# Optimization experiments

Measured on AMD Instinct MI355X. Metric: run time of the kernel, lower is better.

## Reference

```python
import jax, jax.numpy as jnp
from jax import lax
import numpy as np

B, CIN, COUT, H, W = 16, 128, 256, 64, 64
E, K, RED = 4, 3, 4

def setup_inputs() -> dict:
    key = jax.random.key(0)
    ks = jax.random.split(key, 16)
    s = 0.05
    return {
        'x': jax.random.normal(ks[0], (B, CIN, H, W), jnp.float32),
        'expert_w': jax.random.normal(ks[1], (E, COUT, CIN, K, K), jnp.float32) * s,
        'r1_w': jax.random.normal(ks[2], (E // 2, CIN), jnp.float32) * s,
        'r1_b': jnp.zeros((E // 2,), jnp.float32),
        'r2_w': jax.random.normal(ks[3], (E, E // 2), jnp.float32) * s,
        'r2_b': jnp.zeros((E,), jnp.float32),
        'r3_w': jax.random.normal(ks[4], (E, E), jnp.float32) * s,
        'r3_b': jnp.zeros((E,), jnp.float32),
        'ca1_w': jax.random.normal(ks[5], (COUT // RED, COUT), jnp.float32) * s,
        'ca1_b': jnp.zeros((COUT // RED,), jnp.float32),
        'ca2_w': jax.random.normal(ks[6], (COUT, COUT // RED), jnp.float32) * s,
        'ca2_b': jnp.zeros((COUT,), jnp.float32),
        'sa_w': jax.random.normal(ks[7], (1, COUT, 7, 7), jnp.float32) * s,
        'sa_b': jnp.zeros((1,), jnp.float32),
        'bn_gamma': jnp.ones((COUT,), jnp.float32),
        'bn_beta': jnp.zeros((COUT,), jnp.float32),
    }

def _conv(x, w, stride, pad):
    return lax.conv_general_dilated(x, w, (stride, stride), [(pad, pad), (pad, pad)],
                                     dimension_numbers=('NCHW', 'OIHW', 'NCHW'))

def reference(x, expert_w, r1_w, r1_b, r2_w, r2_b, r3_w, r3_b,
              ca1_w, ca1_b, ca2_w, ca2_b, sa_w, sa_b, bn_gamma, bn_beta):
    # --- routing: GAP -> 1x1 convs (as matmuls) -> softmax over experts ---
    g = x.mean(axis=(2, 3))                                   # [B, Cin]
    h = jax.nn.relu(g @ r1_w.T + r1_b)
    h = jax.nn.relu(h @ r2_w.T + r2_b)
    rw = jax.nn.softmax(h @ r3_w.T + r3_b, axis=1)            # [B, E]
    # --- all experts as one stacked conv, then weighted combine ---
    w = expert_w.reshape(E * COUT, CIN, K, K)
    y = _conv(x, w, 1, 1)                                     # [B, E*Cout, H, W]
    y = y.reshape(x.shape[0], E, COUT, y.shape[2], y.shape[3])
    out = jnp.einsum('be,bechw->bchw', rw, y)                 # [B, Cout, H, W]
    # --- channel attention (SE) ---
    p = out.mean(axis=(2, 3))                                  # [B, Cout]
    ca = jax.nn.sigmoid(jax.nn.relu(p @ ca1_w.T + ca1_b) @ ca2_w.T + ca2_b)
    # --- spatial attention: 7x7 conv -> sigmoid ---
    sa = jax.nn.sigmoid(_conv(out, sa_w, 1, 3) + sa_b[None, :, None, None])  # [B,1,H,W]
    out = out * ca[:, :, None, None] * sa
    # --- BatchNorm (training mode: batch statistics) + ReLU ---
    mean = out.mean(axis=(0, 2, 3))
    var = out.var(axis=(0, 2, 3))
    out = (out - mean[None, :, None, None]) * lax.rsqrt(var + 1e-5)[None, :, None, None]
    out = out * bn_gamma[None, :, None, None] + bn_beta[None, :, None, None]
    return jax.nn.relu(out)
```

## Files before the change

kernel.cpp:

```cpp
#include <hip/hip_runtime.h>
#include <math.h>

#define B_    16
#define CIN_  128
#define COUT_ 256
#define H_    64
#define W_    64
#define HW_   4096

typedef __attribute__((ext_vector_type(8))) short short8v;
typedef __attribute__((ext_vector_type(4))) float f32x4;

#define WS_GPX     0
#define WS_RW      131072
#define WS_CP      131136
#define WS_CA      196672
#define WS_BNSCALE 208960
#define WS_BNSHIFT 209216
#define WS_SA      209472
#define WS_WSA     275008
#define WS_WCB_F   283200
#define WS_XT_F    2642496
#define WS_U_F     WS_XT_F
#define WS_MIX_F   7103040

static __device__ __forceinline__ unsigned short f2bf(float f) {
    union { float f; unsigned int u; } v; v.f = f;
    unsigned int u = v.u;
    return (unsigned short)((u + 0x7FFFu + ((u >> 16) & 1u)) >> 16);
}
static __device__ __forceinline__ float bf2f(unsigned short h) {
    union { unsigned int u; float f; } v; v.u = ((unsigned int)h) << 16;
    return v.f;
}

__device__ __forceinline__ void gl16(const void* g, const void* l) {
    __builtin_amdgcn_global_load_lds(
        (const __attribute__((address_space(1))) unsigned int*)g,
        (__attribute__((address_space(3))) unsigned int*)l, 16, 0, 0);
}

__global__ __launch_bounds__(256) void k_xt(const float* __restrict__ x,
                                            unsigned short* __restrict__ xt,
                                            float* __restrict__ gpart) {
    int wg = blockIdx.x + (blockIdx.y << 6);
    int nw = ((wg & 7) << 7) + (wg >> 3);
    int h = nw & 63, b = nw >> 6;
    int t = threadIdx.x;
    int w = t & 63, c8 = t >> 6;
    unsigned short* xtb = xt + (size_t)b * 66*66*128;
    unsigned short* orow = xtb + (((size_t)(h+1))*66 + (w+1))*128;
    float* gp = gpart + ((size_t)b*64 + h)*128;
    #pragma unroll
    for (int i = 0; i < 4; ++i) {
        int ci0 = i*32 + c8*8;
        float f[8];
        short8v vv;
        #pragma unroll
        for (int j = 0; j < 8; ++j) {
            f[j] = x[(((size_t)b*CIN_ + ci0 + j)*H_ + h)*W_ + w];
            vv[j] = (short)f2bf(f[j]);
        }
        *(short8v*)(orow + ci0) = vv;
        #pragma unroll
        for (int j = 0; j < 8; ++j) {
            float s = f[j];
            s += __shfl_down(s, 32, 64);
            s += __shfl_down(s, 16, 64);
            s += __shfl_down(s, 8, 64);
            s += __shfl_down(s, 4, 64);
            s += __shfl_down(s, 2, 64);
            s += __shfl_down(s, 1, 64);
            f[j] = s;
        }
        if (w == 0) {
            #pragma unroll
            for (int j = 0; j < 8; ++j) gp[ci0 + j] = f[j];
        }
    }
    xtb[(((size_t)(h+1))*66 + (t >> 7)*65)*128 + (t & 127)] = 0;
    if (h == 0 || h == 63) {
        int r = (h == 0) ? 0 : 65;
        unsigned short* rowp = xtb + ((size_t)r*66)*128;
        for (int i = t; i < 1056; i += 256)
            *(short8v*)(rowp + (size_t)i*8) = (short8v){0,0,0,0,0,0,0,0};
    }
}

__global__ void k_route(const float* __restrict__ gpart,
                        const float* r1w, const float* r1b,
                        const float* r2w, const float* r2b,
                        const float* r3w, const float* r3b,
                        float* __restrict__ rw) {
    int b = blockIdx.x;
    int t = threadIdx.x;
    __shared__ float gl_[128];
    float s = 0.f;
    for (int h = 0; h < 64; ++h) s += gpart[((size_t)b*64 + h)*128 + t];
    gl_[t] = s * (1.f/4096.f);
    __syncthreads();
    if (t == 0) {
        float h1[2];
        for (int j = 0; j < 2; ++j) {
            float acc = r1b[j];
            for (int c = 0; c < CIN_; ++c) acc += gl_[c]*r1w[j*CIN_+c];
            h1[j] = fmaxf(acc, 0.f);
        }
        float h2[4];
        for (int e = 0; e < 4; ++e)
            h2[e] = fmaxf(r2b[e] + h1[0]*r2w[e*2] + h1[1]*r2w[e*2+1], 0.f);
        float lg[4], m = -1e30f;
        for (int e = 0; e < 4; ++e) {
            float acc = r3b[e];
            for (int j = 0; j < 4; ++j) acc += h2[j]*r3w[e*4+j];
            lg[e] = acc; m = fmaxf(m, acc);
        }
        float den = 0.f;
        for (int e = 0; e < 4; ++e) { lg[e] = expf(lg[e]-m); den += lg[e]; }
        float inv = 1.f/den;
        for (int e = 0; e < 4; ++e) rw[b*4+e] = lg[e]*inv;
    }
}

__global__ __launch_bounds__(256) void k_wcomb(const float* __restrict__ ew,
                                               const float* __restrict__ rw,
                                               unsigned short* __restrict__ wc,
                                               const float* __restrict__ saw,
                                               unsigned short* __restrict__ wsa) {
    int t = threadIdx.x;
    if (blockIdx.x >= COUT_) {
        int i = (blockIdx.x - COUT_)*256 + t;
        int tap = i >> 8, c = i & 255;
        float v = (tap < 49) ? saw[c*49 + tap] : 0.f;
        wsa[tap*256 + c] = f2bf(v);
        return;
    }
    int co = blockIdx.x;
    __shared__ float ewl[4*1152];
    __shared__ float rwl[64];
    #pragma unroll
    for (int e = 0; e < 4; ++e) {
        const float* src = ew + ((size_t)(e*COUT_ + co))*1152;
        for (int i = t; i < 1152; i += 256) ewl[e*1152 + i] = src[i];
    }
    if (t < 64) rwl[t] = rw[t];
    __syncthreads();
    for (int i = 0; i < 72; ++i) {
        int f = i*256 + t;
        int b = f / 1152;
        int rem = f - b*1152;
        int tap = rem >> 7, ci = rem & 127;
        int lidx = ci*9 + tap;
        float v = rwl[b*4+0]*ewl[0*1152+lidx] + rwl[b*4+1]*ewl[1*1152+lidx]
                + rwl[b*4+2]*ewl[2*1152+lidx] + rwl[b*4+3]*ewl[3*1152+lidx];
        wc[((size_t)(b*9 + tap)*COUT_ + co)*128 + ci] = f2bf(v);
    }
}

__global__ __launch_bounds__(256) void k_conv(const unsigned short* __restrict__ xt,
                                              const unsigned short* __restrict__ wc,
                                              unsigned short* __restrict__ mixb,
                                              float* __restrict__ cpart) {
    __shared__ __align__(16) unsigned short xs[1600*8];
    __shared__ __align__(16) unsigned short wl[2304*8];
    __shared__ float gsl[4][64];
    int wg = blockIdx.x + (blockIdx.y << 4) + (blockIdx.z << 6);
    int nw = ((wg & 7) << 7) + (wg >> 3);
    int ht = nw & 15;
    int cb = (nw >> 4) & 3;
    int b  = nw >> 6;
    int t  = threadIdx.x;
    int wv = t >> 6, lane = t & 63;
    int lr = lane & 15, kq = lane >> 4;
    int h0 = ht * 4;

    const unsigned short* xtb = xt + (size_t)b * 66*66*128;
    const unsigned short* wcb = wc + (size_t)b * 9*256*128;

    const char* xs_c = (const char*)xs;
    const char* wl_c = (const char*)wl;
    int base_x = wv*4224 + kq*1056 + lr*16;
    int base_w = kq*1024 + lr*16;

    f32x4 acc[4][4];
    #pragma unroll
    for (int m = 0; m < 4; ++m)
        #pragma unroll
        for (int n = 0; n < 4; ++n) acc[m][n] = (f32x4){0.f,0.f,0.f,0.f};

    for (int ci0 = 0; ci0 < CIN_; ci0 += 32) {
        __syncthreads();
        for (int j = wv; j < 25; j += 4) {
            int s = j*64 + lane;
            if (s > 1583) s = 1583;
            int row = s / 264;
            int rem = s - row*264;
            int kq2 = rem / 66, col = rem - kq2*66;
            const unsigned short* g = xtb + (((size_t)(h0 + row)*66 + col)*128 + ci0 + kq2*8);
            gl16(g, (const char*)xs + (size_t)j*1024);
        }
        for (int j = wv; j < 36; j += 4) {
            int s = j*64 + lane;
            int tap = s >> 8, kq2 = (s >> 6) & 3, co = s & 63;
            const unsigned short* g = wcb + (((size_t)tap*COUT_ + cb*64 + co)*128 + ci0 + kq2*8);
            gl16(g, (const char*)wl + (size_t)j*1024);
        }
        asm volatile("s_waitcnt vmcnt(0)" ::: "memory");
        __syncthreads();

        #pragma unroll
        for (int dh = 0; dh < 3; ++dh) {
            #pragma unroll
            for (int dw = 0; dw < 3; ++dw) {
                int tap = dh*3 + dw;
                short8v af[4], bfv[4];
                #pragma unroll
                for (int m = 0; m < 4; ++m)
                    af[m] = *(const short8v*)(wl_c + base_w + tap*4096 + m*256);
                #pragma unroll
                for (int n = 0; n < 4; ++n)
                    bfv[n] = *(const short8v*)(xs_c + base_x + dh*4224 + dw*16 + n*256);
                #pragma unroll
                for (int m = 0; m < 4; ++m)
                    #pragma unroll
                    for (int n = 0; n < 4; ++n)
                        acc[m][n] = __builtin_amdgcn_mfma_f32_16x16x32_bf16(
                            af[m], bfv[n], acc[m][n], 0, 0, 0);
            }
        }
    }

    unsigned short* ob = mixb + ((size_t)b*COUT_ + cb*64)*HW_ + (h0 + wv)*W_;
    #pragma unroll
    for (int m = 0; m < 4; ++m)
        #pragma unroll
        for (int n = 0; n < 4; ++n) {
            f32x4 v = acc[m][n];
            #pragma unroll
            for (int r = 0; r < 4; ++r)
                ob[(size_t)(m*16 + kq*4 + r)*HW_ + n*16 + lr] = f2bf(v[r]);
        }

    float gp[4][4];
    #pragma unroll
    for (int m = 0; m < 4; ++m)
        #pragma unroll
        for (int r = 0; r < 4; ++r)
            gp[m][r] = acc[m][0][r] + acc[m][1][r] + acc[m][2][r] + acc[m][3][r];
    #pragma unroll
    for (int o = 8; o > 0; o >>= 1)
        #pragma unroll
        for (int m = 0; m < 4; ++m)
            #pragma unroll
            for (int r = 0; r < 4; ++r)
                gp[m][r] += __shfl_down(gp[m][r], o, 64);
    if ((lane & 15) == 0) {
        #pragma unroll
        for (int m = 0; m < 4; ++m)
            #pragma unroll
            for (int r = 0; r < 4; ++r)
                gsl[wv][m*16 + kq*4 + r] = gp[m][r];
    }
    __syncthreads();
    if (t < 64) {
        float s = gsl[0][t] + gsl[1][t] + gsl[2][t] + gsl[3][t];
        cpart[((size_t)b*16 + ht)*COUT_ + cb*64 + t] = s;
    }
}

__global__ __launch_bounds__(256) void k_sa_gemm(const unsigned short* __restrict__ mixb,
                                                 const unsigned short* __restrict__ wsa,
                                                 unsigned short* __restrict__ u) {
    __shared__ unsigned short wl[16384];
    __shared__ unsigned short bt[16384];
    int wg = blockIdx.x + (blockIdx.y << 6);
    int nw = ((wg & 7) << 7) + (wg >> 3);
    int pxt = nw & 63;
    int b   = nw >> 6;
    int t = threadIdx.x, wv = t >> 6, lane = t & 63;
    int lr = lane & 15, kq = lane >> 4;
    int px0 = pxt * 64;

    #pragma unroll
    for (int k = 0; k < 8; ++k) {
        int s = t + k*256;
        int row = s >> 5, cs = s & 31;
        short8v v = *(const short8v*)(wsa + row*256 + cs*8);
        int off = row*512 + ((cs*16) ^ ((row & 7) << 4));
        *(short8v*)((char*)wl + off) = v;
    }
    {
        int px = lane;
        const unsigned short* mb = mixb + (size_t)b*COUT_*HW_ + px0 + px;
        #pragma unroll
        for (int c8 = 0; c8 < 8; ++c8) {
            int cb = wv*64 + c8*8;
            short8v v;
            #pragma unroll
            for (int j = 0; j < 8; ++j)
                v[j] = (short)mb[(size_t)(cb + j)*HW_];
            int off = px*512 + ((cb*2) ^ ((px & 7) << 4));
            *(short8v*)((char*)bt + off) = v;
        }
    }
    __syncthreads();

    f32x4 acc[4];
    #pragma unroll
    for (int n = 0; n < 4; ++n) acc[n] = (f32x4){0.f,0.f,0.f,0.f};

    #pragma unroll
    for (int ks = 0; ks < 8; ++ks) {
        int ci0 = ks*32;
        int arow = wv*16 + lr;
        short8v a = *(const short8v*)((const char*)wl +
                        arow*512 + (((ci0 + kq*8)*2) ^ ((arow & 7) << 4)));
        #pragma unroll
        for (int n = 0; n < 4; ++n) {
            int prow = n*16 + lr;
            short8v bv = *(const short8v*)((const char*)bt +
                            prow*512 + (((ci0 + kq*8)*2) ^ ((prow & 7) << 4)));
            acc[n] = __builtin_amdgcn_mfma_f32_16x16x32_bf16(a, bv, acc[n], 0, 0, 0);
        }
    }

    unsigned short* ub = u + (size_t)b*64*HW_;
    #pragma unroll
    for (int n = 0; n < 4; ++n)
        #pragma unroll
        for (int r = 0; r < 4; ++r)
            ub[(size_t)(wv*16 + kq*4 + r)*HW_ + px0 + n*16 + lr] = f2bf(acc[n][r]);
}

__global__ void k_sared_ca(const unsigned short* __restrict__ u, const float* __restrict__ sab,
                           float* __restrict__ sa,
                           const float* __restrict__ cpart,
                           const float* __restrict__ ca1w, const float* __restrict__ ca1b,
                           const float* __restrict__ ca2w, const float* __restrict__ ca2b,
                           float* __restrict__ ca) {
    int wg = blockIdx.x + (blockIdx.y << 4);
    int nw = ((wg & 7) << 5) + (wg >> 3);
    int hg = nw & 15;
    int b  = nw >> 4;
    int t = threadIdx.x;
    {
        int h = hg * 4 + (t >> 6);
        int w = t & 63;
        float s = sab[0];
        const unsigned short* ub = u + (size_t)b*64*HW_;
        #pragma unroll
        for (int dh = 0; dh < 7; ++dh) {
            int hh = h + dh - 3;
            if (hh < 0 || hh >= H_) continue;
            #pragma unroll
            for (int dw = 0; dw < 7; ++dw) {
                int ww = w + dw - 3;
                if (ww < 0 || ww >= W_) continue;
                s += bf2f(ub[(size_t)(dh*7 + dw)*HW_ + hh*W_ + ww]);
            }
        }
        sa[(size_t)b*HW_ + h*W_ + w] = 1.f/(1.f + expf(-s));
    }
    if (hg == 0) {
        __shared__ float pfull[256];
        __shared__ float h1[64];
        float s0 = 0.f;
        for (int h = 0; h < 16; ++h) s0 += cpart[((size_t)b*16 + h)*COUT_ + t];
        pfull[t] = s0 * (1.f/(float)HW_);
        __syncthreads();
        if (t < 64) {
            float s = ca1b[t];
            for (int c = 0; c < COUT_; ++c) s += pfull[c] * ca1w[t*COUT_ + c];
            h1[t] = fmaxf(s, 0.f);
        }
        __syncthreads();
        float s2 = ca2b[t];
        for (int j = 0; j < 64; ++j) s2 += h1[j] * ca2w[t*64 + j];
        ca[b*COUT_ + t] = 1.f/(1.f + expf(-s2));
    }
}

__global__ void k_statsfin(const unsigned short* __restrict__ mixb,
                           const float* __restrict__ ca, const float* __restrict__ sa,
                           const float* __restrict__ gamma, const float* __restrict__ beta,
                           float* __restrict__ scale, float* __restrict__ shift) {
    int c = blockIdx.x;
    int t = threadIdx.x;
    float s = 0.f, sq = 0.f;
    for (int b = 0; b < B_; ++b) {
        float cav = ca[b*COUT_ + c];
        const unsigned short* pl = mixb + ((size_t)b*COUT_ + c) * HW_;
        const float* sab = sa + (size_t)b * HW_;
        for (int i = t; i < HW_/8; i += 256) {
            short8v v = ((const short8v*)pl)[i];
            float4 w0 = ((const float4*)sab)[2*i];
            float4 w1 = ((const float4*)sab)[2*i+1];
            float f0 = bf2f((unsigned short)v[0])*cav*w0.x;
            float f1 = bf2f((unsigned short)v[1])*cav*w0.y;
            float f2 = bf2f((unsigned short)v[2])*cav*w0.z;
            float f3 = bf2f((unsigned short)v[3])*cav*w0.w;
            float f4 = bf2f((unsigned short)v[4])*cav*w1.x;
            float f5 = bf2f((unsigned short)v[5])*cav*w1.y;
            float f6 = bf2f((unsigned short)v[6])*cav*w1.z;
            float f7 = bf2f((unsigned short)v[7])*cav*w1.w;
            s  += f0+f1+f2+f3+f4+f5+f6+f7;
            sq += f0*f0+f1*f1+f2*f2+f3*f3+f4*f4+f5*f5+f6*f6+f7*f7;
        }
    }
    for (int o = 32; o > 0; o >>= 1) { s += __shfl_down(s,o,64); sq += __shfl_down(sq,o,64); }
    __shared__ float ls[8];
    int wid = t >> 6, lane = t & 63;
    if (lane == 0) { ls[wid] = s; ls[4+wid] = sq; }
    __syncthreads();
    if (t == 0) {
        float ts = ls[0]+ls[1]+ls[2]+ls[3];
        float tq = ls[4]+ls[5]+ls[6]+ls[7];
        float n = (float)(B_*HW_);
        float mean = ts/n;
        float var = tq/n - mean*mean;
        float sc = gamma[c] * rsqrtf(var + 1e-5f);
        scale[c] = sc;
        shift[c] = beta[c] - mean*sc;
    }
}

__global__ void k_bnapply(const unsigned short* __restrict__ mixb, float* __restrict__ out,
                          const float* __restrict__ ca, const float* __restrict__ sa,
                          const float* __restrict__ scale, const float* __restrict__ shift) {
    int wg = blockIdx.x;
    int nw = ((wg & 7) << 10) + (wg >> 3);
    size_t i = (size_t)nw * 256 + threadIdx.x;
    int c = (int)((i >> 9) & 255);
    int b = (int)(i >> 17);
    int px8 = (int)(i & 511);
    float cav = ca[b*COUT_ + c];
    float sc = scale[c], sh = shift[c];
    short8v v = ((const short8v*)mixb)[i];
    const float4* sp = (const float4*)(sa + (size_t)b*HW_) + (size_t)px8*2;
    float4 w0 = sp[0], w1 = sp[1];
    float4 o0, o1;
    o0.x = fmaxf(fmaf(bf2f((unsigned short)v[0])*cav*w0.x, sc, sh), 0.f);
    o0.y = fmaxf(fmaf(bf2f((unsigned short)v[1])*cav*w0.y, sc, sh), 0.f);
    o0.z = fmaxf(fmaf(bf2f((unsigned short)v[2])*cav*w0.z, sc, sh), 0.f);
    o0.w = fmaxf(fmaf(bf2f((unsigned short)v[3])*cav*w0.w, sc, sh), 0.f);
    o1.x = fmaxf(fmaf(bf2f((unsigned short)v[4])*cav*w1.x, sc, sh), 0.f);
    o1.y = fmaxf(fmaf(bf2f((unsigned short)v[5])*cav*w1.y, sc, sh), 0.f);
    o1.z = fmaxf(fmaf(bf2f((unsigned short)v[6])*cav*w1.z, sc, sh), 0.f);
    o1.w = fmaxf(fmaf(bf2f((unsigned short)v[7])*cav*w1.w, sc, sh), 0.f);
    ((float4*)out)[i*2]   = o0;
    ((float4*)out)[i*2+1] = o1;
}

extern "C" void kernel_launch(void* const* d_in, const int* in_sizes, int n_in,
                              void* d_out, int out_size, void* d_ws, size_t ws_size,
                              hipStream_t stream) {
    const float* x    = (const float*)d_in[0];
    const float* ew   = (const float*)d_in[1];
    const float* r1w  = (const float*)d_in[2];
    const float* r1b  = (const float*)d_in[3];
    const float* r2w  = (const float*)d_in[4];
    const float* r2b  = (const float*)d_in[5];
    const float* r3w  = (const float*)d_in[6];
    const float* r3b  = (const float*)d_in[7];
    const float* ca1w = (const float*)d_in[8];
    const float* ca1b = (const float*)d_in[9];
    const float* ca2w = (const float*)d_in[10];
    const float* ca2b = (const float*)d_in[11];
    const float* saw  = (const float*)d_in[12];
    const float* sab  = (const float*)d_in[13];
    const float* gm   = (const float*)d_in[14];
    const float* bt   = (const float*)d_in[15];
    float* out = (float*)d_out;
    float* ws  = (float*)d_ws;
    unsigned short* wcb  = (unsigned short*)(ws + WS_WCB_F);
    unsigned short* xt   = (unsigned short*)(ws + WS_XT_F);
    unsigned short* wsa  = (unsigned short*)(ws + WS_WSA);
    unsigned short* mixb = (unsigned short*)(ws + WS_MIX_F);
    unsigned short* u    = (unsigned short*)(ws + WS_U_F);

    k_xt<<<dim3(64,16), 256, 0, stream>>>(x, xt, ws+WS_GPX);
    k_route<<<16, 128, 0, stream>>>(ws+WS_GPX, r1w, r1b, r2w, r2b, r3w, r3b, ws+WS_RW);
    k_wcomb<<<320, 256, 0, stream>>>(ew, ws+WS_RW, wcb, saw, wsa);
    k_conv<<<dim3(16,4,16), 256, 0, stream>>>(xt, wcb, mixb, ws+WS_CP);
    k_sa_gemm<<<dim3(64,16), 256, 0, stream>>>(mixb, wsa, u);
    k_sared_ca<<<dim3(16,16), 256, 0, stream>>>(u, sab, ws+WS_SA, ws+WS_CP,
                                                ca1w, ca1b, ca2w, ca2b, ws+WS_CA);
    k_statsfin<<<256, 256, 0, stream>>>(mixb, ws+WS_CA, ws+WS_SA, gm, bt,
                                        ws+WS_BNSCALE, ws+WS_BNSHIFT);
    k_bnapply<<<8192, 256, 0, stream>>>(mixb, out, ws+WS_CA, ws+WS_SA,
                                        ws+WS_BNSCALE, ws+WS_BNSHIFT);
}
```

Measured before the change: 144.4 us.

## Restructure conv as double-buffered 256x256 tile GEMM with 8 waves

The implicit-GEMM conv kernel now uses 512-thread blocks that each compute all 256 output channels for a 256-pixel tile, iterating over 18 stages (9 taps x 2 halves of Cin). LDS is double-buffered so global-to-LDS loads for stage t+2 are issued while stage t is consumed, with partial vmcnt waits and barrier/setprio interleaving of LDS reads and MFMA. This aims to raise data reuse per block and hide load latency, but it uses about 128KB of LDS and 128 accumulator registers per thread. It also cuts the grid to 256 blocks, which may leave some CUs idle.

```diff
diff --git a/kernel.cpp b/kernel.cpp
--- a/kernel.cpp
+++ b/kernel.cpp
@@ -157,82 +157,140 @@
     }
 }
 
-__global__ __launch_bounds__(256) void k_conv(const unsigned short* __restrict__ xt,
-                                              const unsigned short* __restrict__ wc,
-                                              unsigned short* __restrict__ mixb,
-                                              float* __restrict__ cpart) {
-    __shared__ __align__(16) unsigned short xs[1600*8];
-    __shared__ __align__(16) unsigned short wl[2304*8];
-    __shared__ float gsl[4][64];
-    int wg = blockIdx.x + (blockIdx.y << 4) + (blockIdx.z << 6);
-    int nw = ((wg & 7) << 7) + (wg >> 3);
-    int ht = nw & 15;
-    int cb = (nw >> 4) & 3;
-    int b  = nw >> 6;
-    int t  = threadIdx.x;
-    int wv = t >> 6, lane = t & 63;
+__global__ __launch_bounds__(512, 2) void k_conv(const unsigned short* __restrict__ xt,
+                                                 const unsigned short* __restrict__ wc,
+                                                 unsigned short* __restrict__ mixb,
+                                                 float* __restrict__ cpart) {
+    __shared__ __align__(16) unsigned short lA[32768];
+    __shared__ __align__(16) unsigned short lB[32768];
+    __shared__ float gsl[4][256];
+    int wg = blockIdx.x;
+    int nw = ((wg & 7) << 5) | (wg >> 3);
+    int pxt = nw & 15;
+    int bb  = nw >> 4;
+    int tid = threadIdx.x;
+    int wv = tid >> 6, lane = tid & 63;
     int lr = lane & 15, kq = lane >> 4;
-    int h0 = ht * 4;
-
-    const unsigned short* xtb = xt + (size_t)b * 66*66*128;
-    const unsigned short* wcb = wc + (size_t)b * 9*256*128;
-
-    const char* xs_c = (const char*)xs;
-    const char* wl_c = (const char*)wl;
-    int base_x = wv*4224 + kq*1056 + lr*16;
-    int base_w = kq*1024 + lr*16;
-
-    f32x4 acc[4][4];
-    #pragma unroll
-    for (int m = 0; m < 4; ++m)
+    int wm = wv >> 2, wn = wv & 3;
+
+    const unsigned short* xtb = xt + (size_t)bb * 66*66*128;
+    const unsigned short* wcb = wc + (size_t)bb * 9*256*128;
+
+    int aidx = (wv & 3)*64 + lane;
+    int hrow = pxt*4 + (wv & 3);
+
+    auto STAGE = [&](int tt) {
+        int buf = tt & 1;
+        int tap = tt >> 1, cih = (tt & 1) * 64;
+        int dh = tap / 3, dw = tap - dh*3;
+        const unsigned short* asrc = wcb + ((size_t)tap*256 + aidx)*128 + cih;
+        const unsigned short* bsrc = xtb + (((size_t)(hrow + dh))*66 + lane + dw)*128 + cih;
+        #pragma unroll
+        for (int q = 0; q < 4; ++q) {
+            int kg = q*2 + (wv >> 2);
+            gl16(asrc + kg*8, (char*)lA + buf*32768 + q*8192 + wv*1024);
+            gl16(bsrc + kg*8, (char*)lB + buf*32768 + q*8192 + wv*1024);
+        }
+    };
+
+    f32x4 acc[8][4];
+    #pragma unroll
+    for (int m = 0; m < 8; ++m)
         #pragma unroll
         for (int n = 0; n < 4; ++n) acc[m][n] = (f32x4){0.f,0.f,0.f,0.f};
 
-    for (int ci0 = 0; ci0 < CIN_; ci0 += 32) {
-        __syncthreads();
-        for (int j = wv; j < 25; j += 4) {
-            int s = j*64 + lane;
-            if (s > 1583) s = 1583;
-            int row = s / 264;
-            int rem = s - row*264;
-            int kq2 = rem / 66, col = rem - kq2*66;
-            const unsigned short* g = xtb + (((size_t)(h0 + row)*66 + col)*128 + ci0 + kq2*8);
-            gl16(g, (const char*)xs + (size_t)j*1024);
-        }
-        for (int j = wv; j < 36; j += 4) {
-            int s = j*64 + lane;
-            int tap = s >> 8, kq2 = (s >> 6) & 3, co = s & 63;
-            const unsigned short* g = wcb + (((size_t)tap*COUT_ + cb*64 + co)*128 + ci0 + kq2*8);
-            gl16(g, (const char*)wl + (size_t)j*1024);
-        }
-        asm volatile("s_waitcnt vmcnt(0)" ::: "memory");
-        __syncthreads();
-
-        #pragma unroll
-        for (int dh = 0; dh < 3; ++dh) {
-            #pragma unroll
-            for (int dw = 0; dw < 3; ++dw) {
-                int tap = dh*3 + dw;
-                short8v af[4], bfv[4];
+    STAGE(0);
+    STAGE(1);
+    asm volatile("s_waitcnt vmcnt(8)" ::: "memory");
+    __builtin_amdgcn_s_barrier();
+
+    for (int t = 0; t < 18; ++t) {
+        int buf = t & 1;
+        const char* pa = (const char*)lA + buf*32768 + kq*4096 + (wm*128 + lr)*16;
+        const char* pb = (const char*)lB + buf*32768 + kq*4096 + (wn*64 + lr)*16;
+        short8v a[4][2], b0[2][2], b1[2][2];
+
+        #pragma unroll
+        for (int m = 0; m < 4; ++m) {
+            a[m][0] = *(const short8v*)(pa + m*256);
+            a[m][1] = *(const short8v*)(pa + 16384 + m*256);
+        }
+        #pragma unroll
+        for (int n = 0; n < 2; ++n) {
+            b0[n][0] = *(const short8v*)(pb + n*256);
+            b0[n][1] = *(const short8v*)(pb + 16384 + n*256);
+        }
+        __builtin_amdgcn_s_barrier();
+        __builtin_amdgcn_s_setprio(1);
+        #pragma unroll
+        for (int m = 0; m < 4; ++m)
+            #pragma unroll
+            for (int n = 0; n < 2; ++n)
                 #pragma unroll
-                for (int m = 0; m < 4; ++m)
-                    af[m] = *(const short8v*)(wl_c + base_w + tap*4096 + m*256);
+                for (int ks = 0; ks < 2; ++ks)
+                    acc[m][n] = __builtin_amdgcn_mfma_f32_16x16x32_bf16(a[m][ks], b0[n][ks], acc[m][n], 0, 0, 0);
+        __builtin_amdgcn_s_setprio(0);
+        __builtin_amdgcn_s_barrier();
+
+        #pragma unroll
+        for (int n = 0; n < 2; ++n) {
+            b1[n][0] = *(const short8v*)(pb + (2+n)*256);
+            b1[n][1] = *(const short8v*)(pb + 16384 + (2+n)*256);
+        }
+        __builtin_amdgcn_s_barrier();
+        __builtin_amdgcn_s_setprio(1);
+        #pragma unroll
+        for (int m = 0; m < 4; ++m)
+            #pragma unroll
+            for (int n = 0; n < 2; ++n)
                 #pragma unroll
-                for (int n = 0; n < 4; ++n)
-                    bfv[n] = *(const short8v*)(xs_c + base_x + dh*4224 + dw*16 + n*256);
+                for (int ks = 0; ks < 2; ++ks)
+                    acc[m][2+n] = __builtin_amdgcn_mfma_f32_16x16x32_bf16(a[m][ks], b1[n][ks], acc[m][2+n], 0, 0, 0);
+        __builtin_amdgcn_s_setprio(0);
+        __builtin_amdgcn_s_barrier();
+
+        #pragma unroll
+        for (int m = 0; m < 4; ++m) {
+            a[m][0] = *(const short8v*)(pa + (4+m)*256);
+            a[m][1] = *(const short8v*)(pa + 16384 + (4+m)*256);
+        }
+        __builtin_amdgcn_s_barrier();
+        __builtin_amdgcn_s_setprio(1);
+        #pragma unroll
+        for (int m = 0; m < 4; ++m)
+            #pragma unroll
+            for (int n = 0; n < 2; ++n)
                 #pragma unroll
-                for (int m = 0; m < 4; ++m)
-                    #pragma unroll
-                    for (int n = 0; n < 4; ++n)
-                        acc[m][n] = __builtin_amdgcn_mfma_f32_16x16x32_bf16(
-                            af[m], bfv[n], acc[m][n], 0, 0, 0);
-            }
-        }
-    }
-
-    unsigned short* ob = mixb + ((size_t)b*COUT_ + cb*64)*HW_ + (h0 + wv)*W_;
-    #pragma unroll
-    for (int m = 0; m < 4; ++m)
+                for (int ks = 0; ks < 2; ++ks)
+                    acc[4+m][n] = __builtin_amdgcn_mfma_f32_16x16x32_bf16(a[m][ks], b0[n][ks], acc[4+m][n], 0, 0, 0);
+        __builtin_amdgcn_s_setprio(0);
+        __builtin_amdgcn_s_barrier();
+
+        __builtin_amdgcn_s_barrier();
+        __builtin_amdgcn_s_setprio(1);
+        #pragma unroll
+        for (int m = 0; m < 4; ++m)
+            #pragma unroll
+            for (int n = 0; n < 2; ++n)
+                #pragma unroll
+                for (int ks = 0; ks < 2; ++ks)
+                    acc[4+m][2+n] = __builtin_amdgcn_mfma_f32_16x16x32_bf16(a[m][ks], b1[n][ks], acc[4+m][2+n], 0, 0, 0);
+        __builtin_amdgcn_s_setprio(0);
+        __builtin_amdgcn_s_barrier();
+
+        __builtin_amdgcn_sched_barrier(0);
+        if (t < 16) {
+            STAGE(t + 2);
+            asm volatile("s_waitcnt vmcnt(8)" ::: "memory");
+        } else {
+            asm volatile("s_waitcnt vmcnt(0)" ::: "memory");
+        }
+        __builtin_amdgcn_s_barrier();
+    }
+
+    unsigned short* ob = mixb + ((size_t)bb*COUT_ + wm*128)*HW_ + pxt*256 + wn*64;
+    #pragma unroll
+    for (int m = 0; m < 8; ++m)
         #pragma unroll
         for (int n = 0; n < 4; ++n) {
             f32x4 v = acc[m][n];
@@ -241,30 +299,27 @@
                 ob[(size_t)(m*16 + kq*4 + r)*HW_ + n*16 + lr] = f2bf(v[r]);
         }
 
-    float gp[4][4];
-    #pragma unroll
-    for (int m = 0; m < 4; ++m)
-        #pragma unroll
-        for (int r = 0; r < 4; ++r)
-            gp[m][r] = acc[m][0][r] + acc[m][1][r] + acc[m][2][r] + acc[m][3][r];
-    #pragma unroll
-    for (int o = 8; o > 0; o >>= 1)
-        #pragma unroll
-        for (int m = 0; m < 4; ++m)
+    float gp[8][4];
+    #pragma unroll
+    for (int m = 0; m < 8; ++m)
+        #pragma unroll
+        for (int r = 0; r < 4; ++r) {
+            float s = acc[m][0][r] + acc[m][1][r] + acc[m][2][r] + acc[m][3][r];
+            #pragma unroll
+            for (int o = 8; o > 0; o >>= 1) s += __shfl_down(s, o, 64);
+            gp[m][r] = s;
+        }
+    if (lr == 0) {
+        #pragma unroll
+        for (int m = 0; m < 8; ++m)
             #pragma unroll
             for (int r = 0; r < 4; ++r)
-                gp[m][r] += __shfl_down(gp[m][r], o, 64);
-    if ((lane & 15) == 0) {
-        #pragma unroll
-        for (int m = 0; m < 4; ++m)
-            #pragma unroll
-            for (int r = 0; r < 4; ++r)
-                gsl[wv][m*16 + kq*4 + r] = gp[m][r];
+                gsl[wn][wm*128 + m*16 + kq*4 + r] = gp[m][r];
     }
     __syncthreads();
-    if (t < 64) {
-        float s = gsl[0][t] + gsl[1][t] + gsl[2][t] + gsl[3][t];
-        cpart[((size_t)b*16 + ht)*COUT_ + cb*64 + t] = s;
+    if (tid < 256) {
+        float s = gsl[0][tid] + gsl[1][tid] + gsl[2][tid] + gsl[3][tid];
+        cpart[((size_t)bb*16 + pxt)*COUT_ + tid] = s;
     }
 }
 
@@ -481,7 +536,7 @@
     k_xt<<<dim3(64,16), 256, 0, stream>>>(x, xt, ws+WS_GPX);
     k_route<<<16, 128, 0, stream>>>(ws+WS_GPX, r1w, r1b, r2w, r2b, r3w, r3b, ws+WS_RW);
     k_wcomb<<<320, 256, 0, stream>>>(ew, ws+WS_RW, wcb, saw, wsa);
-    k_conv<<<dim3(16,4,16), 256, 0, stream>>>(xt, wcb, mixb, ws+WS_CP);
+    k_conv<<<256, 512, 0, stream>>>(xt, wcb, mixb, ws+WS_CP);
     k_sa_gemm<<<dim3(64,16), 256, 0, stream>>>(mixb, wsa, u);
     k_sared_ca<<<dim3(16,16), 256, 0, stream>>>(u, sab, ws+WS_SA, ws+WS_CP,
                                                 ca1w, ca1b, ca2w, ca2b, ws+WS_CA);
```

New measurement: 200.1 us. +38.5%, slower.
